# Optimization experiments

Measured on AMD Instinct MI355X. Metric: run time of the kernel, lower is better.

Reference implementation:

```python
import jax, jax.numpy as jnp
import numpy as np

NUM_HEADS = 16
EPS = 1e-5


def _layernorm(x, gamma, beta):
    # LayerNorm over last dim (head_dim), biased variance as in torch
    mu = jnp.mean(x, axis=-1, keepdims=True)
    var = jnp.mean(jnp.square(x - mu), axis=-1, keepdims=True)
    return (x - mu) * jax.lax.rsqrt(var + EPS) * gamma + beta


def setup_inputs() -> dict:
    key = jax.random.key(0)
    ks = jax.random.split(key, 10)
    B, T, C = 16, 2048, 1024
    Bk = 4
    Dh = C // NUM_HEADS
    w = 0.02
    return {
        "q": jax.random.normal(ks[0], (B, T, C), jnp.float32),
        "k": jax.random.normal(ks[1], (Bk, T, C), jnp.float32),
        "v": jax.random.normal(ks[2], (Bk, T, C), jnp.float32),
        "Wq": jax.random.normal(ks[3], (C, C), jnp.float32) * w,
        "Wk": jax.random.normal(ks[4], (C, C), jnp.float32) * w,
        "Wv": jax.random.normal(ks[5], (C, C), jnp.float32) * w,
        "Wo": jax.random.normal(ks[6], (C, C), jnp.float32) * w,
        "bo": jnp.zeros((C,), jnp.float32),
        "gamma": jnp.ones((Dh,), jnp.float32),
        "beta": jnp.zeros((Dh,), jnp.float32),
    }


def reference(q, k, v, Wq, Wk, Wv, Wo, bo, gamma, beta):
    B, N, C = q.shape
    H = NUM_HEADS
    Dh = C // H
    scale = 8.0 / Dh  # use_mup=True

    reps = B // k.shape[0]
    k = jnp.tile(k, (reps, 1, 1))[:, :N]
    v = jnp.tile(v, (reps, 1, 1))[:, :N]

    # torch Linear: x @ W.T  (no qkv bias)
    qp = jnp.einsum("bnc,dc->bnd", q, Wq).reshape(B, N, H, Dh)
    kp = jnp.einsum("bnc,dc->bnd", k, Wk).reshape(B, N, H, Dh)
    vp = jnp.einsum("bnc,dc->bnd", v, Wv).reshape(B, N, H, Dh)

    qp = _layernorm(qp, gamma, beta) * scale
    kp = _layernorm(kp, gamma, beta)

    # Faithful to source: NO head permute before matmul -> per-token (H,H) attention
    attn = jnp.einsum("bnhd,bngd->bnhg", qp, kp)  # [B,N,H,H]
    attn = jax.nn.softmax(attn, axis=-1)
    x = jnp.einsum("bnhg,bngd->bnhd", attn, vp)  # [B,N,H,Dh]
    # torch: transpose(1,2).reshape(B,N,C)
    x = x.transpose(0, 2, 1, 3).reshape(B, N, C)
    return jnp.einsum("bnc,dc->bnd", x, Wo) + bo
```

## Files before the change

### kernel.cpp

```cpp
#include <hip/hip_runtime.h>
#include <stdint.h>

typedef short bf16x8 __attribute__((ext_vector_type(8)));
typedef float f32x4 __attribute__((ext_vector_type(4)));

#define DEVINL static __device__ __forceinline__
#define SB() __builtin_amdgcn_sched_barrier(0)

DEVINL unsigned short f2bf(float f) {
    union { float f; uint32_t u; } v; v.f = f;
    return (unsigned short)((v.u + 0x7FFFu + ((v.u >> 16) & 1u)) >> 16);
}
DEVINL float bf2f(unsigned short b) {
    union { uint32_t u; float f; } v; v.u = ((uint32_t)b) << 16;
    return v.f;
}

DEVINL void load_lds16(const void* g, void* l) {
    __builtin_amdgcn_global_load_lds(
        (const __attribute__((address_space(1))) void*)g,
        (__attribute__((address_space(3))) void*)l, 16, 0, 0);
}

__global__ __launch_bounds__(256) void k_cvt(const float* __restrict__ src,
                                             unsigned short* __restrict__ dst, int n4) {
    int stride = gridDim.x * blockDim.x;
    for (int i = blockIdx.x * blockDim.x + threadIdx.x; i < n4; i += stride) {
        float4 f = reinterpret_cast<const float4*>(src)[i];
        ushort4 o;
        o.x = f2bf(f.x); o.y = f2bf(f.y); o.z = f2bf(f.z); o.w = f2bf(f.w);
        reinterpret_cast<ushort4*>(dst)[i] = o;
    }
}

__global__ __launch_bounds__(256) void k_cvt2(
    const float* __restrict__ s0, const float* __restrict__ s1,
    unsigned short* __restrict__ d0, unsigned short* __restrict__ d1, int n4) {
    const int half = gridDim.x >> 1;
    const int sel = blockIdx.x < half ? 0 : 1;
    const float* src = sel ? s1 : s0;
    unsigned short* dst = sel ? d1 : d0;
    const int blk = blockIdx.x - sel * half;
    for (int i = blk * 256 + threadIdx.x; i < n4; i += half * 256) {
        float4 f = reinterpret_cast<const float4*>(src)[i];
        ushort4 o;
        o.x = f2bf(f.x); o.y = f2bf(f.y); o.z = f2bf(f.z); o.w = f2bf(f.w);
        reinterpret_cast<ushort4*>(dst)[i] = o;
    }
}

__global__ __launch_bounds__(256) void k_cvtW(
    const float* __restrict__ s0, const float* __restrict__ s1,
    const float* __restrict__ s2, const float* __restrict__ s3,
    unsigned short* __restrict__ d0, unsigned short* __restrict__ d1,
    unsigned short* __restrict__ d2, unsigned short* __restrict__ d3) {
    const float* srcs[4] = {s0, s1, s2, s3};
    unsigned short* dsts[4] = {d0, d1, d2, d3};
    const int wsel = blockIdx.x >> 8;
    const int blk  = blockIdx.x & 255;
    const float* src = srcs[wsel];
    unsigned short* dst = dsts[wsel];
    for (int i = blk * 256 + threadIdx.x; i < 262144; i += 65536) {
        float4 f = reinterpret_cast<const float4*>(src)[i];
        ushort4 o;
        o.x = f2bf(f.x); o.y = f2bf(f.y); o.z = f2bf(f.z); o.w = f2bf(f.w);
        reinterpret_cast<ushort4*>(dst)[i] = o;
    }
}

#define LOFF(buf, ab, ks, row) (((((buf) * 2 + (ab)) * 2 + (ks)) * 256 + (row)) * 32)

template<int EPI>
DEVINL void gemm256_body(
    const unsigned short* __restrict__ A,
    const unsigned short* __restrict__ B,
    void* __restrict__ Cout,
    const float* __restrict__ bias,
    const float* __restrict__ gamma,
    const float* __restrict__ beta,
    unsigned short* lds, int bid, int nwg, int tid)
{
    constexpr int K = 1024;
    constexpr int N = 1024;
    constexpr int NT = 16;

    const int wg  = (bid & 7) * (nwg >> 3) + (bid >> 3);
    const int m0 = (wg >> 2) * 256;
    const int n0 = (wg & 3) * 256;

    const int w = tid >> 6;
    const int lane = tid & 63;
    const int wr = w >> 2;
    const int wc = w & 3;

    const int srow = lane >> 2;
    const int sseg = lane & 3;
    const int sslot = sseg ^ ((srow >> 1) & 3);

    f32x4 acc[8][4] = {};

    auto stage_unit = [&](int buf, int kt, int unit) {
        const int k0 = kt * 64;
        const int ab = unit & 1;
        const int sel = unit >> 1;
        #pragma unroll
        for (int j = 0; j < 2; ++j) {
            const int c  = (w << 1) | j;
            const int ks = c >> 3;
            const int c3 = c & 7;
            const int rg = ab ? (sel * 2 + (c3 & 1) + ((c3 >> 1) << 2))
                              : (sel * 4 + (c3 & 3) + ((c3 >> 2) << 3));
            const int row = rg * 16 + srow;
            const unsigned short* src =
                (ab ? B + (size_t)(n0 + row) * K : A + (size_t)(m0 + row) * K)
                + k0 + ks * 32 + sslot * 8;
            load_lds16(src, lds + LOFF(buf, ab, ks, rg * 16));
        }
    };

    const int rr = lane & 15;
    const int rdslot = ((lane >> 4) ^ ((rr >> 1) & 3)) * 8;

    stage_unit(0, 0, 0);
    stage_unit(0, 0, 1);
    stage_unit(0, 0, 2);
    stage_unit(0, 0, 3);

    bf16x8 a[4][2], b0[2][2], b1[2][2];
    int cur = 0;
    for (int kt = 0; kt < NT - 1; ++kt) {
        const int nxt = cur ^ 1;

        stage_unit(nxt, kt + 1, 0);
        asm volatile("s_waitcnt vmcnt(6)" ::: "memory");
        __builtin_amdgcn_s_barrier();
        SB();
        #pragma unroll
        for (int i = 0; i < 4; ++i)
            #pragma unroll
            for (int ks = 0; ks < 2; ++ks)
                a[i][ks] = *reinterpret_cast<const bf16x8*>(
                    lds + LOFF(cur, 0, ks, wr * 128 + i * 16 + rr) + rdslot);
        #pragma unroll
        for (int j = 0; j < 2; ++j)
            #pragma unroll
            for (int ks = 0; ks < 2; ++ks)
                b0[j][ks] = *reinterpret_cast<const bf16x8*>(
                    lds + LOFF(cur, 1, ks, wc * 64 + j * 16 + rr) + rdslot);
        asm volatile("s_waitcnt lgkmcnt(0)" ::: "memory");
        SB();
        __builtin_amdgcn_s_setprio(1);
        #pragma unroll
        for (int i = 0; i < 4; ++i)
            #pragma unroll
            for (int j = 0; j < 2; ++j)
                #pragma unroll
                for (int ks = 0; ks < 2; ++ks)
                    acc[i][j] = __builtin_amdgcn_mfma_f32_16x16x32_bf16(
                        a[i][ks], b0[j][ks], acc[i][j], 0, 0, 0);
        __builtin_amdgcn_s_setprio(0);

        stage_unit(nxt, kt + 1, 1);
        asm volatile("s_waitcnt vmcnt(4)" ::: "memory");
        __builtin_amdgcn_s_barrier();
        SB();
        #pragma unroll
        for (int j = 0; j < 2; ++j)
            #pragma unroll
            for (int ks = 0; ks < 2; ++ks)
                b1[j][ks] = *reinterpret_cast<const bf16x8*>(
                    lds + LOFF(cur, 1, ks, wc * 64 + 32 + j * 16 + rr) + rdslot);
        asm volatile("s_waitcnt lgkmcnt(0)" ::: "memory");
        SB();
        __builtin_amdgcn_s_setprio(1);
        #pragma unroll
        for (int i = 0; i < 4; ++i)
            #pragma unroll
            for (int j = 0; j < 2; ++j)
                #pragma unroll
                for (int ks = 0; ks < 2; ++ks)
                    acc[i][2 + j] = __builtin_amdgcn_mfma_f32_16x16x32_bf16(
                        a[i][ks], b1[j][ks], acc[i][2 + j], 0, 0, 0);
        __builtin_amdgcn_s_setprio(0);

        stage_unit(nxt, kt + 1, 2);
        __builtin_amdgcn_s_barrier();
        SB();
        #pragma unroll
        for (int i = 0; i < 4; ++i)
            #pragma unroll
            for (int ks = 0; ks < 2; ++ks)
                a[i][ks] = *reinterpret_cast<const bf16x8*>(
                    lds + LOFF(cur, 0, ks, wr * 128 + 64 + i * 16 + rr) + rdslot);
        asm volatile("s_waitcnt lgkmcnt(0)" ::: "memory");
        SB();
        __builtin_amdgcn_s_setprio(1);
        #pragma unroll
        for (int i = 0; i < 4; ++i)
            #pragma unroll
            for (int j = 0; j < 2; ++j)
                #pragma unroll
                for (int ks = 0; ks < 2; ++ks)
                    acc[4 + i][j] = __builtin_amdgcn_mfma_f32_16x16x32_bf16(
                        a[i][ks], b0[j][ks], acc[4 + i][j], 0, 0, 0);
        __builtin_amdgcn_s_setprio(0);

        stage_unit(nxt, kt + 1, 3);
        __builtin_amdgcn_s_barrier();
        SB();
        __builtin_amdgcn_s_setprio(1);
        #pragma unroll
        for (int i = 0; i < 4; ++i)
            #pragma unroll
            for (int j = 0; j < 2; ++j)
                #pragma unroll
                for (int ks = 0; ks < 2; ++ks)
                    acc[4 + i][2 + j] = __builtin_amdgcn_mfma_f32_16x16x32_bf16(
                        a[i][ks], b1[j][ks], acc[4 + i][2 + j], 0, 0, 0);
        __builtin_amdgcn_s_setprio(0);
        cur = nxt;
    }

    {
        asm volatile("s_waitcnt vmcnt(4)" ::: "memory");
        __builtin_amdgcn_s_barrier();
        SB();
        #pragma unroll
        for (int i = 0; i < 4; ++i)
            #pragma unroll
            for (int ks = 0; ks < 2; ++ks)
                a[i][ks] = *reinterpret_cast<const bf16x8*>(
                    lds + LOFF(cur, 0, ks, wr * 128 + i * 16 + rr) + rdslot);
        #pragma unroll
        for (int j = 0; j < 2; ++j)
            #pragma unroll
            for (int ks = 0; ks < 2; ++ks)
                b0[j][ks] = *reinterpret_cast<const bf16x8*>(
                    lds + LOFF(cur, 1, ks, wc * 64 + j * 16 + rr) + rdslot);
        asm volatile("s_waitcnt lgkmcnt(0)" ::: "memory");
        SB();
        __builtin_amdgcn_s_setprio(1);
        #pragma unroll
        for (int i = 0; i < 4; ++i)
            #pragma unroll
            for (int j = 0; j < 2; ++j)
                #pragma unroll
                for (int ks = 0; ks < 2; ++ks)
                    acc[i][j] = __builtin_amdgcn_mfma_f32_16x16x32_bf16(
                        a[i][ks], b0[j][ks], acc[i][j], 0, 0, 0);
        __builtin_amdgcn_s_setprio(0);

        asm volatile("s_waitcnt vmcnt(0)" ::: "memory");
        __builtin_amdgcn_s_barrier();
        SB();
        #pragma unroll
        for (int j = 0; j < 2; ++j)
            #pragma unroll
            for (int ks = 0; ks < 2; ++ks)
                b1[j][ks] = *reinterpret_cast<const bf16x8*>(
                    lds + LOFF(cur, 1, ks, wc * 64 + 32 + j * 16 + rr) + rdslot);
        asm volatile("s_waitcnt lgkmcnt(0)" ::: "memory");
        SB();
        __builtin_amdgcn_s_setprio(1);
        #pragma unroll
        for (int i = 0; i < 4; ++i)
            #pragma unroll
            for (int j = 0; j < 2; ++j)
                #pragma unroll
                for (int ks = 0; ks < 2; ++ks)
                    acc[i][2 + j] = __builtin_amdgcn_mfma_f32_16x16x32_bf16(
                        a[i][ks], b1[j][ks], acc[i][2 + j], 0, 0, 0);
        __builtin_amdgcn_s_setprio(0);

        #pragma unroll
        for (int i = 0; i < 4; ++i)
            #pragma unroll
            for (int ks = 0; ks < 2; ++ks)
                a[i][ks] = *reinterpret_cast<const bf16x8*>(
                    lds + LOFF(cur, 0, ks, wr * 128 + 64 + i * 16 + rr) + rdslot);
        asm volatile("s_waitcnt lgkmcnt(0)" ::: "memory");
        SB();
        __builtin_amdgcn_s_setprio(1);
        #pragma unroll
        for (int i = 0; i < 4; ++i)
            #pragma unroll
            for (int j = 0; j < 2; ++j)
                #pragma unroll
                for (int ks = 0; ks < 2; ++ks) {
                    acc[4 + i][j] = __builtin_amdgcn_mfma_f32_16x16x32_bf16(
                        a[i][ks], b0[j][ks], acc[4 + i][j], 0, 0, 0);
                    acc[4 + i][2 + j] = __builtin_amdgcn_mfma_f32_16x16x32_bf16(
                        a[i][ks], b1[j][ks], acc[4 + i][2 + j], 0, 0, 0);
                }
        __builtin_amdgcn_s_setprio(0);
    }

    const int rg = lane >> 4;
    if constexpr (EPI == 0) {
        #pragma unroll
        for (int jj = 0; jj < 4; ++jj) {
            const int col = n0 + wc * 64 + jj * 16 + rr;
            const float bv = bias[col];
            #pragma unroll
            for (int i = 0; i < 8; ++i) {
                const int row0 = m0 + wr * 128 + i * 16 + rg * 4;
                #pragma unroll
                for (int r = 0; r < 4; ++r)
                    reinterpret_cast<float*>(Cout)[(size_t)(row0 + r) * N + col] =
                        acc[i][jj][r] + bv;
            }
        }
    } else if constexpr (EPI == 1 || EPI == 3) {
        const float scale = (EPI == 1) ? 0.125f : 1.0f;
        float gm[4], bt[4];
        #pragma unroll
        for (int jj = 0; jj < 4; ++jj) { gm[jj] = gamma[jj * 16 + rr]; bt[jj] = beta[jj * 16 + rr]; }
        #pragma unroll
        for (int i = 0; i < 8; ++i)
            #pragma unroll
            for (int r = 0; r < 4; ++r) {
                float s = 0.f, sq = 0.f;
                #pragma unroll
                for (int jj = 0; jj < 4; ++jj) {
                    const float v = acc[i][jj][r];
                    s += v; sq += v * v;
                }
                s  += __shfl_xor(s, 1);  s  += __shfl_xor(s, 2);
                s  += __shfl_xor(s, 4);  s  += __shfl_xor(s, 8);
                sq += __shfl_xor(sq, 1); sq += __shfl_xor(sq, 2);
                sq += __shfl_xor(sq, 4); sq += __shfl_xor(sq, 8);
                const float mu = s * 0.015625f;
                const float var = sq * 0.015625f - mu * mu;
                const float inv = rsqrtf(var + 1e-5f);
                const int row = m0 + wr * 128 + i * 16 + rg * 4 + r;
                #pragma unroll
                for (int jj = 0; jj < 4; ++jj) {
                    const int col = n0 + wc * 64 + jj * 16 + rr;
                    const float val = ((acc[i][jj][r] - mu) * inv * gm[jj] + bt[jj]) * scale;
                    reinterpret_cast<unsigned short*>(Cout)[(size_t)row * N + col] = f2bf(val);
                }
            }
    } else {
        const int g = (wg & 3) * 4 + wc;
        const int kqv = g >> 3;
        const int ev = g & 7;
        #pragma unroll
        for (int i = 0; i < 8; ++i)
            #pragma unroll
            for (int r = 0; r < 4; ++r) {
                const int t = m0 + wr * 128 + i * 16 + rg * 4 + r;
                #pragma unroll
                for (int jj = 0; jj < 4; ++jj)
                    reinterpret_cast<unsigned short*>(Cout)[
                        (size_t)t * 1024 + jj * 256 + kqv * 128 + rr * 8 + ev] =
                        f2bf(acc[i][jj][r]);
            }
    }
}

template<int EPI>
__global__ __launch_bounds__(512, 2) void k_gemm256(
    const unsigned short* __restrict__ A,
    const unsigned short* __restrict__ B,
    void* __restrict__ Cout,
    const float* __restrict__ bias,
    const float* __restrict__ gamma,
    const float* __restrict__ beta)
{
    __shared__ __align__(16) unsigned short lds[2 * 2 * 2 * 256 * 32];
    gemm256_body<EPI>(A, B, Cout, bias, gamma, beta, lds, blockIdx.x, gridDim.x, threadIdx.x);
}

__global__ __launch_bounds__(512, 2) void k_gemm256kv(
    const unsigned short* __restrict__ Ak,
    const unsigned short* __restrict__ Bk,
    void* __restrict__ Ck,
    const unsigned short* __restrict__ Av,
    const unsigned short* __restrict__ Bv,
    void* __restrict__ Cv,
    const float* __restrict__ gamma,
    const float* __restrict__ beta)
{
    __shared__ __align__(16) unsigned short lds[2 * 2 * 2 * 256 * 32];
    if (blockIdx.x < 128)
        gemm256_body<3>(Ak, Bk, Ck, nullptr, gamma, beta, lds, blockIdx.x, 128, threadIdx.x);
    else
        gemm256_body<2>(Av, Bv, Cv, nullptr, nullptr, nullptr, lds, blockIdx.x - 128, 128, threadIdx.x);
}

__global__ __launch_bounds__(256) void k_attn2(
    const unsigned short* __restrict__ qln,
    const unsigned short* __restrict__ kln,
    const unsigned short* __restrict__ vperm,
    unsigned short* __restrict__ xout)
{
    __shared__ unsigned short ps[4][256];
    __shared__ unsigned short xs[4][16 * 68];

    const int w = threadIdx.x >> 6;
    const int lane = threadIdx.x & 63;
    const int token = blockIdx.x * 4 + w;
    const int b = token >> 11;
    const int n = token & 2047;
    const int tokk = (b & 3) * 2048 + n;
    const int rr = lane & 15;
    const int kq = lane >> 4;

    const unsigned short* qp = qln + (size_t)token * 1024 + rr * 64 + kq * 8;
    const unsigned short* kp = kln + (size_t)tokk * 1024 + rr * 64 + kq * 8;
    const bf16x8 aq0 = *reinterpret_cast<const bf16x8*>(qp);
    const bf16x8 aq1 = *reinterpret_cast<const bf16x8*>(qp + 32);
    const bf16x8 bk0 = *reinterpret_cast<const bf16x8*>(kp);
    const bf16x8 bk1 = *reinterpret_cast<const bf16x8*>(kp + 32);
    f32x4 s = {};
    s = __builtin_amdgcn_mfma_f32_16x16x32_bf16(aq0, bk0, s, 0, 0, 0);
    s = __builtin_amdgcn_mfma_f32_16x16x32_bf16(aq1, bk1, s, 0, 0, 0);

    #pragma unroll
    for (int r = 0; r < 4; ++r) {
        float m = s[r];
        m = fmaxf(m, __shfl_xor(m, 1));
        m = fmaxf(m, __shfl_xor(m, 2));
        m = fmaxf(m, __shfl_xor(m, 4));
        m = fmaxf(m, __shfl_xor(m, 8));
        const float e = __expf(s[r] - m);
        float t = e;
        t += __shfl_xor(t, 1); t += __shfl_xor(t, 2);
        t += __shfl_xor(t, 4); t += __shfl_xor(t, 8);
        ps[w][(kq * 4 + r) * 16 + rr] = f2bf(e / t);
    }

    bf16x8 ap = {};
    if (kq < 2)
        ap = *reinterpret_cast<const bf16x8*>(&ps[w][rr * 16 + kq * 8]);

    const unsigned short* vp = vperm + (size_t)tokk * 1024;
    #pragma unroll
    for (int dblk = 0; dblk < 4; ++dblk) {
        bf16x8 bv = {};
        if (kq < 2)
            bv = *reinterpret_cast<const bf16x8*>(vp + dblk * 256 + kq * 128 + rr * 8);
        f32x4 z = {};
        const f32x4 x = __builtin_amdgcn_mfma_f32_16x16x32_bf16(ap, bv, z, 0, 0, 0);
        #pragma unroll
        for (int r = 0; r < 4; ++r)
            xs[w][(kq * 4 + r) * 68 + dblk * 16 + rr] = f2bf(x[r]);
    }

    const int h2 = lane >> 2;
    const int sg = lane & 3;
    const uint4 lo = *reinterpret_cast<const uint4*>(&xs[w][h2 * 68 + sg * 16]);
    const uint4 hi = *reinterpret_cast<const uint4*>(&xs[w][h2 * 68 + sg * 16 + 8]);
    unsigned short* dst = xout + (size_t)b * 2048 * 1024 +
                          (size_t)(h2 * 128 + (n >> 4)) * 1024 + (n & 15) * 64 + sg * 16;
    *reinterpret_cast<uint4*>(dst) = lo;
    *reinterpret_cast<uint4*>(dst + 8) = hi;
}

extern "C" void kernel_launch(void* const* d_in, const int* in_sizes, int n_in,
                              void* d_out, int out_size, void* d_ws, size_t ws_size,
                              hipStream_t stream) {
    const float* q     = (const float*)d_in[0];
    const float* k     = (const float*)d_in[1];
    const float* v     = (const float*)d_in[2];
    const float* Wq    = (const float*)d_in[3];
    const float* Wk    = (const float*)d_in[4];
    const float* Wv    = (const float*)d_in[5];
    const float* Wo    = (const float*)d_in[6];
    const float* bo    = (const float*)d_in[7];
    const float* gamma = (const float*)d_in[8];
    const float* beta  = (const float*)d_in[9];
    float* out = (float*)d_out;

    char* ws = (char*)d_ws;
    const size_t MB = 1024 * 1024;
    unsigned short* qb    = (unsigned short*)(ws + 0);
    unsigned short* xsc   = (unsigned short*)(ws + 0);
    unsigned short* qpb   = (unsigned short*)(ws + 64 * MB);
    unsigned short* klnb  = (unsigned short*)(ws + 128 * MB);
    unsigned short* vbb   = (unsigned short*)(ws + 144 * MB);
    unsigned short* vpm   = (unsigned short*)(ws + 160 * MB);
    unsigned short* kbb   = (unsigned short*)(ws + 176 * MB);
    unsigned short* Wkb   = (unsigned short*)(ws + 192 * MB);
    unsigned short* Wvb   = (unsigned short*)(ws + 194 * MB);
    unsigned short* Wqb   = (unsigned short*)(ws + 196 * MB);
    unsigned short* Wob   = (unsigned short*)(ws + 198 * MB);

    k_cvtW<<<1024, 256, 0, stream>>>(Wk, Wv, Wq, Wo, Wkb, Wvb, Wqb, Wob);

    k_cvt2<<<2048, 256, 0, stream>>>(k, v, kbb, vbb, 2097152);

    k_gemm256kv<<<256, 512, 0, stream>>>(kbb, Wkb, klnb, vbb, Wvb, vpm, gamma, beta);

    k_cvt<<<2048, 256, 0, stream>>>(q, qb, 8388608);

    k_gemm256<1><<<512, 512, 0, stream>>>(qb, Wqb, qpb, nullptr, gamma, beta);

    k_attn2<<<8192, 256, 0, stream>>>(qpb, klnb, vpm, xsc);

    k_gemm256<0><<<512, 512, 0, stream>>>(xsc, Wob, out, bo, nullptr, nullptr);
}
```

Before: 310.0 us.

## Reorder GEMM main loop to issue LDS reads before staging and barriers

Restructures the 256x256 bf16 GEMM main loop so LDS fragment reads for each quadrant are issued before the next tile's global-to-LDS stage and before the barrier. It also reorders the stage units (3 before 2) and moves the initial wait and barrier into the prologue. The goal is to overlap LDS read latency with global load issue and barrier waits, shortening stalls between MFMA blocks. The risk is subtle hazards from the changed vmcnt counts and barrier placement when buffers are reused.

```diff
diff --git a/kernel.cpp b/kernel.cpp
--- a/kernel.cpp
+++ b/kernel.cpp
@@ -121,179 +121,115 @@
     const int rr = lane & 15;
     const int rdslot = ((lane >> 4) ^ ((rr >> 1) & 3)) * 8;
 
+    auto rd_a = [&](bf16x8 (&dst)[4][2], int cur, int mh) {
+        #pragma unroll
+        for (int i = 0; i < 4; ++i)
+            #pragma unroll
+            for (int ks = 0; ks < 2; ++ks)
+                dst[i][ks] = *reinterpret_cast<const bf16x8*>(
+                    lds + LOFF(cur, 0, ks, wr * 128 + mh * 64 + i * 16 + rr) + rdslot);
+    };
+    auto rd_b = [&](bf16x8 (&dst)[2][2], int cur, int nh) {
+        #pragma unroll
+        for (int j = 0; j < 2; ++j)
+            #pragma unroll
+            for (int ks = 0; ks < 2; ++ks)
+                dst[j][ks] = *reinterpret_cast<const bf16x8*>(
+                    lds + LOFF(cur, 1, ks, wc * 64 + nh * 32 + j * 16 + rr) + rdslot);
+    };
+
+    #define MFMA_QUAD(mi, nj, av, bv)                                          \
+        __builtin_amdgcn_s_setprio(1);                                         \
+        _Pragma("unroll")                                                      \
+        for (int i = 0; i < 4; ++i)                                            \
+            _Pragma("unroll")                                                  \
+            for (int j = 0; j < 2; ++j)                                        \
+                _Pragma("unroll")                                              \
+                for (int ks = 0; ks < 2; ++ks)                                 \
+                    acc[(mi) * 4 + i][(nj) * 2 + j] =                          \
+                        __builtin_amdgcn_mfma_f32_16x16x32_bf16(               \
+                            av[i][ks], bv[j][ks], acc[(mi)*4+i][(nj)*2+j], 0, 0, 0); \
+        __builtin_amdgcn_s_setprio(0);
+
     stage_unit(0, 0, 0);
     stage_unit(0, 0, 1);
+    stage_unit(0, 0, 3);
     stage_unit(0, 0, 2);
-    stage_unit(0, 0, 3);
+    asm volatile("s_waitcnt vmcnt(4)" ::: "memory");
+    __builtin_amdgcn_s_barrier();
+    SB();
 
     bf16x8 a[4][2], b0[2][2], b1[2][2];
     int cur = 0;
     for (int kt = 0; kt < NT - 1; ++kt) {
         const int nxt = cur ^ 1;
 
+        rd_a(a, cur, 0);
+        rd_b(b0, cur, 0);
+        SB();
         stage_unit(nxt, kt + 1, 0);
-        asm volatile("s_waitcnt vmcnt(6)" ::: "memory");
-        __builtin_amdgcn_s_barrier();
-        SB();
-        #pragma unroll
-        for (int i = 0; i < 4; ++i)
-            #pragma unroll
-            for (int ks = 0; ks < 2; ++ks)
-                a[i][ks] = *reinterpret_cast<const bf16x8*>(
-                    lds + LOFF(cur, 0, ks, wr * 128 + i * 16 + rr) + rdslot);
-        #pragma unroll
-        for (int j = 0; j < 2; ++j)
-            #pragma unroll
-            for (int ks = 0; ks < 2; ++ks)
-                b0[j][ks] = *reinterpret_cast<const bf16x8*>(
-                    lds + LOFF(cur, 1, ks, wc * 64 + j * 16 + rr) + rdslot);
-        asm volatile("s_waitcnt lgkmcnt(0)" ::: "memory");
-        SB();
-        __builtin_amdgcn_s_setprio(1);
-        #pragma unroll
-        for (int i = 0; i < 4; ++i)
-            #pragma unroll
-            for (int j = 0; j < 2; ++j)
-                #pragma unroll
-                for (int ks = 0; ks < 2; ++ks)
-                    acc[i][j] = __builtin_amdgcn_mfma_f32_16x16x32_bf16(
-                        a[i][ks], b0[j][ks], acc[i][j], 0, 0, 0);
-        __builtin_amdgcn_s_setprio(0);
-
+        asm volatile("s_waitcnt vmcnt(4)" ::: "memory");
+        __builtin_amdgcn_s_barrier();
+        SB();
+        asm volatile("s_waitcnt lgkmcnt(0)" ::: "memory");
+        SB();
+        MFMA_QUAD(0, 0, a, b0)
+
+        rd_b(b1, cur, 1);
+        SB();
         stage_unit(nxt, kt + 1, 1);
         asm volatile("s_waitcnt vmcnt(4)" ::: "memory");
         __builtin_amdgcn_s_barrier();
         SB();
-        #pragma unroll
-        for (int j = 0; j < 2; ++j)
-            #pragma unroll
-            for (int ks = 0; ks < 2; ++ks)
-                b1[j][ks] = *reinterpret_cast<const bf16x8*>(
-                    lds + LOFF(cur, 1, ks, wc * 64 + 32 + j * 16 + rr) + rdslot);
-        asm volatile("s_waitcnt lgkmcnt(0)" ::: "memory");
-        SB();
-        __builtin_amdgcn_s_setprio(1);
-        #pragma unroll
-        for (int i = 0; i < 4; ++i)
-            #pragma unroll
-            for (int j = 0; j < 2; ++j)
-                #pragma unroll
-                for (int ks = 0; ks < 2; ++ks)
-                    acc[i][2 + j] = __builtin_amdgcn_mfma_f32_16x16x32_bf16(
-                        a[i][ks], b1[j][ks], acc[i][2 + j], 0, 0, 0);
-        __builtin_amdgcn_s_setprio(0);
+        asm volatile("s_waitcnt lgkmcnt(0)" ::: "memory");
+        SB();
+        MFMA_QUAD(0, 1, a, b1)
+
+        rd_a(a, cur, 1);
+        SB();
+        stage_unit(nxt, kt + 1, 3);
+        __builtin_amdgcn_s_barrier();
+        SB();
+        asm volatile("s_waitcnt lgkmcnt(0)" ::: "memory");
+        SB();
+        MFMA_QUAD(1, 0, a, b0)
 
         stage_unit(nxt, kt + 1, 2);
-        __builtin_amdgcn_s_barrier();
-        SB();
-        #pragma unroll
-        for (int i = 0; i < 4; ++i)
-            #pragma unroll
-            for (int ks = 0; ks < 2; ++ks)
-                a[i][ks] = *reinterpret_cast<const bf16x8*>(
-                    lds + LOFF(cur, 0, ks, wr * 128 + 64 + i * 16 + rr) + rdslot);
-        asm volatile("s_waitcnt lgkmcnt(0)" ::: "memory");
-        SB();
-        __builtin_amdgcn_s_setprio(1);
-        #pragma unroll
-        for (int i = 0; i < 4; ++i)
-            #pragma unroll
-            for (int j = 0; j < 2; ++j)
-                #pragma unroll
-                for (int ks = 0; ks < 2; ++ks)
-                    acc[4 + i][j] = __builtin_amdgcn_mfma_f32_16x16x32_bf16(
-                        a[i][ks], b0[j][ks], acc[4 + i][j], 0, 0, 0);
-        __builtin_amdgcn_s_setprio(0);
-
-        stage_unit(nxt, kt + 1, 3);
-        __builtin_amdgcn_s_barrier();
-        SB();
-        __builtin_amdgcn_s_setprio(1);
-        #pragma unroll
-        for (int i = 0; i < 4; ++i)
-            #pragma unroll
-            for (int j = 0; j < 2; ++j)
-                #pragma unroll
-                for (int ks = 0; ks < 2; ++ks)
-                    acc[4 + i][2 + j] = __builtin_amdgcn_mfma_f32_16x16x32_bf16(
-                        a[i][ks], b1[j][ks], acc[4 + i][2 + j], 0, 0, 0);
-        __builtin_amdgcn_s_setprio(0);
+        asm volatile("s_waitcnt vmcnt(4)" ::: "memory");
+        __builtin_amdgcn_s_barrier();
+        SB();
+        MFMA_QUAD(1, 1, a, b1)
         cur = nxt;
     }
 
     {
-        asm volatile("s_waitcnt vmcnt(4)" ::: "memory");
-        __builtin_amdgcn_s_barrier();
-        SB();
-        #pragma unroll
-        for (int i = 0; i < 4; ++i)
-            #pragma unroll
-            for (int ks = 0; ks < 2; ++ks)
-                a[i][ks] = *reinterpret_cast<const bf16x8*>(
-                    lds + LOFF(cur, 0, ks, wr * 128 + i * 16 + rr) + rdslot);
-        #pragma unroll
-        for (int j = 0; j < 2; ++j)
-            #pragma unroll
-            for (int ks = 0; ks < 2; ++ks)
-                b0[j][ks] = *reinterpret_cast<const bf16x8*>(
-                    lds + LOFF(cur, 1, ks, wc * 64 + j * 16 + rr) + rdslot);
-        asm volatile("s_waitcnt lgkmcnt(0)" ::: "memory");
-        SB();
-        __builtin_amdgcn_s_setprio(1);
-        #pragma unroll
-        for (int i = 0; i < 4; ++i)
-            #pragma unroll
-            for (int j = 0; j < 2; ++j)
-                #pragma unroll
-                for (int ks = 0; ks < 2; ++ks)
-                    acc[i][j] = __builtin_amdgcn_mfma_f32_16x16x32_bf16(
-                        a[i][ks], b0[j][ks], acc[i][j], 0, 0, 0);
-        __builtin_amdgcn_s_setprio(0);
-
+        rd_a(a, cur, 0);
+        rd_b(b0, cur, 0);
+        SB();
+        asm volatile("s_waitcnt vmcnt(2)" ::: "memory");
+        __builtin_amdgcn_s_barrier();
+        SB();
+        asm volatile("s_waitcnt lgkmcnt(0)" ::: "memory");
+        SB();
+        MFMA_QUAD(0, 0, a, b0)
+
+        rd_b(b1, cur, 1);
+        SB();
         asm volatile("s_waitcnt vmcnt(0)" ::: "memory");
         __builtin_amdgcn_s_barrier();
         SB();
-        #pragma unroll
-        for (int j = 0; j < 2; ++j)
-            #pragma unroll
-            for (int ks = 0; ks < 2; ++ks)
-                b1[j][ks] = *reinterpret_cast<const bf16x8*>(
-                    lds + LOFF(cur, 1, ks, wc * 64 + 32 + j * 16 + rr) + rdslot);
-        asm volatile("s_waitcnt lgkmcnt(0)" ::: "memory");
-        SB();
-        __builtin_amdgcn_s_setprio(1);
-        #pragma unroll
-        for (int i = 0; i < 4; ++i)
-            #pragma unroll
-            for (int j = 0; j < 2; ++j)
-                #pragma unroll
-                for (int ks = 0; ks < 2; ++ks)
-                    acc[i][2 + j] = __builtin_amdgcn_mfma_f32_16x16x32_bf16(
-                        a[i][ks], b1[j][ks], acc[i][2 + j], 0, 0, 0);
-        __builtin_amdgcn_s_setprio(0);
-
-        #pragma unroll
-        for (int i = 0; i < 4; ++i)
-            #pragma unroll
-            for (int ks = 0; ks < 2; ++ks)
-                a[i][ks] = *reinterpret_cast<const bf16x8*>(
-                    lds + LOFF(cur, 0, ks, wr * 128 + 64 + i * 16 + rr) + rdslot);
-        asm volatile("s_waitcnt lgkmcnt(0)" ::: "memory");
-        SB();
-        __builtin_amdgcn_s_setprio(1);
-        #pragma unroll
-        for (int i = 0; i < 4; ++i)
-            #pragma unroll
-            for (int j = 0; j < 2; ++j)
-                #pragma unroll
-                for (int ks = 0; ks < 2; ++ks) {
-                    acc[4 + i][j] = __builtin_amdgcn_mfma_f32_16x16x32_bf16(
-                        a[i][ks], b0[j][ks], acc[4 + i][j], 0, 0, 0);
-                    acc[4 + i][2 + j] = __builtin_amdgcn_mfma_f32_16x16x32_bf16(
-                        a[i][ks], b1[j][ks], acc[4 + i][2 + j], 0, 0, 0);
-                }
-        __builtin_amdgcn_s_setprio(0);
-    }
+        asm volatile("s_waitcnt lgkmcnt(0)" ::: "memory");
+        SB();
+        MFMA_QUAD(0, 1, a, b1)
+
+        rd_a(a, cur, 1);
+        SB();
+        asm volatile("s_waitcnt lgkmcnt(0)" ::: "memory");
+        SB();
+        MFMA_QUAD(1, 0, a, b0)
+        MFMA_QUAD(1, 1, a, b1)
+    }
+    #undef MFMA_QUAD
 
     const int rg = lane >> 4;
     if constexpr (EPI == 0) {
```

Result: no change. 307.9 us (-0.7%).
